# Performance work log

Hardware: AMD Instinct MI355X
Metric: run time of the kernel (lower is better)

Reference implementation:

```python
import jax, jax.numpy as jnp
import numpy as np

LEAK = 0.1
LOG_2PI = float(np.log(2.0 * np.pi))


def setup_inputs() -> dict:
    key = jax.random.key(0)
    k1, k2, k3, k4 = jax.random.split(key, 4)
    B, S, K = 128, 8192, 16
    obvs = jax.random.normal(k1, (B, S, 1), dtype=jnp.float32)
    mu = jax.random.normal(k2, (K,), dtype=jnp.float32)
    log_sigma = 0.1 * jax.random.normal(k3, (K,), dtype=jnp.float32)
    prior_logits = jax.random.normal(k4, (K,), dtype=jnp.float32)
    return {"obvs": obvs, "mu": mu, "log_sigma": log_sigma, "prior_logits": prior_logits}


def _log_transition(num_states: int) -> jnp.ndarray:
    # LeakyTransfer: diagonal-dominant stochastic matrix, stay prob 1-leak,
    # leak mass spread uniformly over the other K-1 states.
    eye = jnp.eye(num_states, dtype=jnp.float32)
    A = (1.0 - LEAK) * eye + (LEAK / (num_states - 1)) * (1.0 - eye)
    return jnp.log(A)


def reference(obvs, mu, log_sigma, prior_logits):
    K = mu.shape[0]
    # Gaussian emission NLL per state: [B, S, K]
    sigma = jnp.exp(log_sigma)
    nll = 0.5 * ((obvs - mu) / sigma) ** 2 + log_sigma + 0.5 * LOG_2PI
    ln_em = -nll  # ln_emission_probs

    log_prior = jax.nn.log_softmax(prior_logits)  # CategoricalPrior
    logA = _log_transition(K)  # [K, K] (from -> to)

    # forward recursion: carry[b, j] = ln_em[b, t, j] + logsumexp_i(carry[b, i] + logA[i, j])
    init = ln_em[:, 0, :] + log_prior  # [B, K]
    em_rest = jnp.swapaxes(ln_em[:, 1:, :], 0, 1)  # [S-1, B, K]

    def step(carry, em_t):
        trans = jax.nn.logsumexp(carry[:, :, None] + logA[None, :, :], axis=1)  # [B, K]
        carry = em_t + trans
        return carry, None

    final, _ = jax.lax.scan(step, init, em_rest)
    return jnp.sum(jax.nn.logsumexp(final, axis=-1))
```

## Files before the change

### kernel.cpp

```cpp
#include <hip/hip_runtime.h>

#define NB 128
#define NS 8192
#define NC 128
#define NCP 64
#define NL (NS / NC)
#define M4 (NL / 4)

#define LOG2E 1.4426950408889634f
#define HLOG2PI 0.918938533204672742f
#define LN2 0.69314718055994531f

#define ROWS 20
#define UNIT 640
#define SLOT 320

__device__ __forceinline__ float fexp2(float x) { return __builtin_amdgcn_exp2f(x); }
__device__ __forceinline__ float flog2(float x) { return __builtin_amdgcn_logf(x); }

__device__ __forceinline__ float gsum16(float v) {
    v += __shfl_xor(v, 1, 16);
    v += __shfl_xor(v, 2, 16);
    v += __shfl_xor(v, 4, 16);
    v += __shfl_xor(v, 8, 16);
    return v;
}
__device__ __forceinline__ float gmax16(float v) {
    v = fmaxf(v, __shfl_xor(v, 1, 16));
    v = fmaxf(v, __shfl_xor(v, 2, 16));
    v = fmaxf(v, __shfl_xor(v, 4, 16));
    v = fmaxf(v, __shfl_xor(v, 8, 16));
    return v;
}

template <int K>
__device__ __forceinline__ int rotk(int x) {
    return __builtin_amdgcn_mov_dpp(x, 0x120 + K, 0xF, 0xF, true);
}

__device__ __forceinline__ float step2(float (&W)[16], float T, float xx,
                                       float A2, float B2, float C2) {
    const float amb = 0.9f - 0.1f / 15.0f;
    const float bco = 0.1f / 15.0f;
    float myl = fexp2(fmaf(xx, fmaf(xx, A2, B2), C2));
    int mi = __float_as_int(myl);
    float bT = bco * T;
    W[0]  = fmaf(amb, W[0],  bT) * myl;
    W[1]  = fmaf(amb, W[1],  bT) * __int_as_float(rotk<1>(mi));
    W[2]  = fmaf(amb, W[2],  bT) * __int_as_float(rotk<2>(mi));
    W[3]  = fmaf(amb, W[3],  bT) * __int_as_float(rotk<3>(mi));
    W[4]  = fmaf(amb, W[4],  bT) * __int_as_float(rotk<4>(mi));
    W[5]  = fmaf(amb, W[5],  bT) * __int_as_float(rotk<5>(mi));
    W[6]  = fmaf(amb, W[6],  bT) * __int_as_float(rotk<6>(mi));
    W[7]  = fmaf(amb, W[7],  bT) * __int_as_float(rotk<7>(mi));
    W[8]  = fmaf(amb, W[8],  bT) * __int_as_float(rotk<8>(mi));
    W[9]  = fmaf(amb, W[9],  bT) * __int_as_float(rotk<9>(mi));
    W[10] = fmaf(amb, W[10], bT) * __int_as_float(rotk<10>(mi));
    W[11] = fmaf(amb, W[11], bT) * __int_as_float(rotk<11>(mi));
    W[12] = fmaf(amb, W[12], bT) * __int_as_float(rotk<12>(mi));
    W[13] = fmaf(amb, W[13], bT) * __int_as_float(rotk<13>(mi));
    W[14] = fmaf(amb, W[14], bT) * __int_as_float(rotk<14>(mi));
    W[15] = fmaf(amb, W[15], bT) * __int_as_float(rotk<15>(mi));
    float s0 = (W[0] + W[1]) + (W[2] + W[3]);
    float s1 = (W[4] + W[5]) + (W[6] + W[7]);
    float s2 = (W[8] + W[9]) + (W[10] + W[11]);
    float s3 = (W[12] + W[13]) + (W[14] + W[15]);
    return (s0 + s1) + (s2 + s3);
}

__global__ __launch_bounds__(256, 4) void hmm_phase1(const float* __restrict__ obvs,
                                                     const float* __restrict__ mu,
                                                     const float* __restrict__ log_sigma,
                                                     float* __restrict__ wsW,
                                                     float* __restrict__ wsM,
                                                     float* __restrict__ out) {
    __shared__ float lds[16 * UNIT];
    int tid = blockIdx.x * 256 + threadIdx.x;
    if (tid == 0) out[0] = 0.0f;
    int r = threadIdx.x & 15;
    int u = threadIdx.x >> 4;
    int g = tid >> 4;
    int b = g >> 7;
    int c = g & (NC - 1);

    float ls = log_sigma[r];
    float mk = mu[r];
    float iv = fexp2(-2.0f * LOG2E * ls);
    float A2 = -0.5f * LOG2E * iv;
    float B2 = LOG2E * mk * iv;
    float C2 = LOG2E * (-0.5f * mk * mk * iv - ls - HLOG2PI);

    float W[16];
#pragma unroll
    for (int k = 0; k < 16; ++k) W[k] = (k == 0) ? 1.0f : 0.0f;
    int ilog = 0;
    float T = 1.0f;

    const float4* ob4 = (const float4*)(obvs + (long)b * NS) + c * M4;
    float4 xv = ob4[0];
    float4 xn = ob4[1];
    if (c) T = step2(W, T, xv.x, A2, B2, C2);
    T = step2(W, T, xv.y, A2, B2, C2);
    T = step2(W, T, xv.z, A2, B2, C2);
    T = step2(W, T, xv.w, A2, B2, C2);
    {
        int te = (__float_as_int(T) >> 23) & 255;
        int ok = (te != 0);
        float s = ok ? __int_as_float((254 - te) << 23) : 1.0f;
        ilog += ok ? (te - 127) : 0;
#pragma unroll
        for (int k = 0; k < 16; ++k) W[k] *= s;
        T *= s;
    }
    xv = xn;
    for (int m = 1; m < M4; ++m) {
        xn = ob4[(m + 1) < M4 ? (m + 1) : m];
        T = step2(W, T, xv.x, A2, B2, C2);
        T = step2(W, T, xv.y, A2, B2, C2);
        T = step2(W, T, xv.z, A2, B2, C2);
        T = step2(W, T, xv.w, A2, B2, C2);
        int te = (__float_as_int(T) >> 23) & 255;
        int ok = (te != 0);
        float s = ok ? __int_as_float((254 - te) << 23) : 1.0f;
        ilog += ok ? (te - 127) : 0;
#pragma unroll
        for (int k = 0; k < 16; ++k) W[k] *= s;
        T *= s;
        xv = xn;
    }

    int sid[16];
    sid[0] = r;
    sid[1]  = rotk<1>(r);   sid[2]  = rotk<2>(r);   sid[3]  = rotk<3>(r);
    sid[4]  = rotk<4>(r);   sid[5]  = rotk<5>(r);   sid[6]  = rotk<6>(r);
    sid[7]  = rotk<7>(r);   sid[8]  = rotk<8>(r);   sid[9]  = rotk<9>(r);
    sid[10] = rotk<10>(r);  sid[11] = rotk<11>(r);  sid[12] = rotk<12>(r);
    sid[13] = rotk<13>(r);  sid[14] = rotk<14>(r);  sid[15] = rotk<15>(r);

    float lg = (float)ilog + flog2(T);
    float mx = gmax16(lg);
    float sc = fexp2((float)ilog - mx);

    float* Ru = lds + u * UNIT;
    float* Tu = lds + u * UNIT + SLOT;
#pragma unroll
    for (int k = 0; k < 16; ++k) {
        float w = W[k] * sc;
        int j = sid[k];
        Ru[j * ROWS + r] = w;
        Tu[r * ROWS + j] = w;
    }
    if (r == 0) Ru[16] = mx;
    __syncthreads();

    int lane = threadIdx.x & 63;
    int wid = threadIdx.x >> 6;
    long p0 = (long)blockIdx.x * 8;
#pragma unroll
    for (int q = 0; q < 2; ++q) {
        int p = 2 * wid + q;
        const float* MbR = lds + (2 * p + 1) * UNIT;
        const float* MaT = lds + (2 * p) * UNIT + SLOT;
        int a = lane >> 3, cc = lane & 7;
        float b0[16], b1[16], a0[16], a1[16];
        const float4* pb0 = (const float4*)(MbR + (2 * a) * ROWS);
        const float4* pb1 = (const float4*)(MbR + (2 * a + 1) * ROWS);
        const float4* pa0 = (const float4*)(MaT + (2 * cc) * ROWS);
        const float4* pa1 = (const float4*)(MaT + (2 * cc + 1) * ROWS);
#pragma unroll
        for (int qq = 0; qq < 4; ++qq) {
            *(float4*)&b0[4 * qq] = pb0[qq];
            *(float4*)&b1[4 * qq] = pb1[qq];
            *(float4*)&a0[4 * qq] = pa0[qq];
            *(float4*)&a1[4 * qq] = pa1[qq];
        }
        float c00 = 0.f, c01 = 0.f, c10 = 0.f, c11 = 0.f;
#pragma unroll
        for (int k = 0; k < 16; ++k) {
            c00 = fmaf(b0[k], a0[k], c00);
            c01 = fmaf(b0[k], a1[k], c01);
            c10 = fmaf(b1[k], a0[k], c10);
            c11 = fmaf(b1[k], a1[k], c11);
        }
        float cs0 = c00 + c10;
        float cs1 = c01 + c11;
        cs0 += __shfl_xor(cs0, 8);  cs1 += __shfl_xor(cs1, 8);
        cs0 += __shfl_xor(cs0, 16); cs1 += __shfl_xor(cs1, 16);
        cs0 += __shfl_xor(cs0, 32); cs1 += __shfl_xor(cs1, 32);
        float mxc = fmaxf(cs0, cs1);
        mxc = fmaxf(mxc, __shfl_xor(mxc, 1));
        mxc = fmaxf(mxc, __shfl_xor(mxc, 2));
        mxc = fmaxf(mxc, __shfl_xor(mxc, 4));
        float is = 1.0f / mxc;
        float* dst = wsW + (p0 + p) * 256;
        *(float2*)(dst + (2 * a) * 16 + 2 * cc)     = make_float2(c00 * is, c01 * is);
        *(float2*)(dst + (2 * a + 1) * 16 + 2 * cc) = make_float2(c10 * is, c11 * is);
        if (lane == 0) {
            float mxa = lds[(2 * p) * UNIT + 16];
            float mxb = lds[(2 * p + 1) * UNIT + 16];
            wsM[p0 + p] = mxa + mxb + flog2(mxc);
        }
    }
}

__device__ __forceinline__ void mat16_mul(float* dR, float* dT,
                                          const float* MbR, const float* MaT,
                                          int lane) {
    int a = lane >> 3;
    int cc = lane & 7;
    float b0[16], b1[16], a0[16], a1[16];
    const float4* pb0 = (const float4*)(MbR + (2 * a) * ROWS);
    const float4* pb1 = (const float4*)(MbR + (2 * a + 1) * ROWS);
    const float4* pa0 = (const float4*)(MaT + (2 * cc) * ROWS);
    const float4* pa1 = (const float4*)(MaT + (2 * cc + 1) * ROWS);
#pragma unroll
    for (int q = 0; q < 4; ++q) {
        *(float4*)&b0[4 * q] = pb0[q];
        *(float4*)&b1[4 * q] = pb1[q];
        *(float4*)&a0[4 * q] = pa0[q];
        *(float4*)&a1[4 * q] = pa1[q];
    }
    float c00 = 0.f, c01 = 0.f, c10 = 0.f, c11 = 0.f;
#pragma unroll
    for (int k = 0; k < 16; ++k) {
        c00 = fmaf(b0[k], a0[k], c00);
        c01 = fmaf(b0[k], a1[k], c01);
        c10 = fmaf(b1[k], a0[k], c10);
        c11 = fmaf(b1[k], a1[k], c11);
    }
    *(float2*)(dR + (2 * a) * ROWS + 2 * cc)     = make_float2(c00, c01);
    *(float2*)(dR + (2 * a + 1) * ROWS + 2 * cc) = make_float2(c10, c11);
    if (dT) {
        *(float2*)(dT + (2 * cc) * ROWS + 2 * a)     = make_float2(c00, c10);
        *(float2*)(dT + (2 * cc + 1) * ROWS + 2 * a) = make_float2(c01, c11);
    }
}

__global__ __launch_bounds__(256, 2) void hmm_phase23(const float* __restrict__ obvs,
                                                      const float* __restrict__ mu,
                                                      const float* __restrict__ log_sigma,
                                                      const float* __restrict__ prior_logits,
                                                      const float* __restrict__ wsW,
                                                      const float* __restrict__ wsM,
                                                      float* __restrict__ out) {
    __shared__ float smem[12800];
    float* stage = smem;
    float* scr   = smem + 5120;
    float* resB  = smem + 10240;

    int bb = blockIdx.x;
    int tid = threadIdx.x;
    int wid = tid >> 6;
    int lane = tid & 63;

    for (int rd = 0; rd < 8; ++rd) {
        const float4* src = (const float4*)(wsW + ((long)bb * NCP + rd * 8) * 256);
        __syncthreads();
#pragma unroll
        for (int q = 0; q < 2; ++q) {
            int f = tid + q * 256;
            float4 v = src[f];
            int m = f >> 6, idx = f & 63, j = idx >> 2, kq = idx & 3;
            *(float4*)(stage + m * UNIT + j * ROWS + kq * 4) = v;
            float* Tb = stage + m * UNIT + SLOT;
            Tb[(4 * kq + 0) * ROWS + j] = v.x;
            Tb[(4 * kq + 1) * ROWS + j] = v.y;
            Tb[(4 * kq + 2) * ROWS + j] = v.z;
            Tb[(4 * kq + 3) * ROWS + j] = v.w;
        }
        __syncthreads();
        if (wid < 4)
            mat16_mul(scr + wid * UNIT, scr + wid * UNIT + SLOT,
                      stage + (2 * wid + 1) * UNIT, stage + (2 * wid) * UNIT + SLOT, lane);
        __syncthreads();
        if (wid < 2)
            mat16_mul(scr + (4 + wid) * UNIT, scr + (4 + wid) * UNIT + SLOT,
                      scr + (2 * wid + 1) * UNIT, scr + (2 * wid) * UNIT + SLOT, lane);
        __syncthreads();
        if (wid == 0)
            mat16_mul(resB + rd * SLOT, nullptr,
                      scr + 5 * UNIT, scr + 4 * UNIT + SLOT, lane);
    }
    __syncthreads();

    for (int e = tid; e < 8 * 256; e += 256) {
        int m = e >> 8, idx = e & 255, j = idx >> 4, r = idx & 15;
        stage[m * SLOT + r * ROWS + j] = resB[m * SLOT + j * ROWS + r];
    }
    __syncthreads();

    for (int i = wid; i < 4; i += 4)
        mat16_mul(scr + i * UNIT, scr + i * UNIT + SLOT,
                  resB + (2 * i + 1) * SLOT, stage + (2 * i) * SLOT, lane);
    __syncthreads();
    float* cur = scr;
    float* oth = stage;
    int n = 4;
    while (n > 1) {
        n >>= 1;
        for (int i = wid; i < n; i += 4)
            mat16_mul(oth + i * UNIT, oth + i * UNIT + SLOT,
                      cur + (2 * i + 1) * UNIT, cur + (2 * i) * UNIT + SLOT, lane);
        __syncthreads();
        float* t = cur; cur = oth; oth = t;
    }

    if (tid < 16) {
        int jj = tid;
        float ls = log_sigma[jj];
        float mk = mu[jj];
        float iv = fexp2(-2.0f * LOG2E * ls);
        float A2 = -0.5f * LOG2E * iv;
        float B2 = LOG2E * mk * iv;
        float C2 = LOG2E * (-0.5f * mk * mk * iv - ls - HLOG2PI);
        float x = obvs[(long)bb * NS];
        float e = fexp2(LOG2E * prior_logits[jj]);
        float Z = gsum16(e);
        float p0 = fexp2(fmaf(x, fmaf(x, A2, B2), C2)) * e;
        const float* Mrow = cur + jj * ROWS;
        float mr[16];
        *(float4*)&mr[0]  = ((const float4*)Mrow)[0];
        *(float4*)&mr[4]  = ((const float4*)Mrow)[1];
        *(float4*)&mr[8]  = ((const float4*)Mrow)[2];
        *(float4*)&mr[12] = ((const float4*)Mrow)[3];
        float q = 0.0f;
#pragma unroll
        for (int rr = 0; rr < 16; ++rr) q = fmaf(mr[rr], __shfl(p0, rr, 16), q);
        float Tq = gsum16(q);
        const float* pm = wsM + bb * NCP + jj * 4;
        float msum = gsum16(pm[0] + pm[1] + pm[2] + pm[3]);
        if (jj == 0) {
            float res = (flog2(Tq) - flog2(Z) + msum) * LN2;
            atomicAdd(out, res);
        }
    }
}

extern "C" void kernel_launch(void* const* d_in, const int* in_sizes, int n_in,
                              void* d_out, int out_size, void* d_ws, size_t ws_size,
                              hipStream_t stream) {
    const float* obvs = (const float*)d_in[0];
    const float* mu = (const float*)d_in[1];
    const float* log_sigma = (const float*)d_in[2];
    const float* prior_logits = (const float*)d_in[3];
    float* out = (float*)d_out;

    float* wsW = (float*)d_ws;
    float* wsM = wsW + (size_t)NB * NCP * 256;

    hmm_phase1<<<dim3(NB * NC * 16 / 256), dim3(256), 0, stream>>>(obvs, mu, log_sigma,
                                                                   wsW, wsM, out);
    hmm_phase23<<<dim3(NB), dim3(256), 0, stream>>>(obvs, mu, log_sigma, prior_logits,
                                                    wsW, wsM, out);
}
```

Measured before the change: 106.4 us.

## Reduce full per-block matrix tree in phase1 to cut phase23 workload

Phase1 now combines all 16 per-chunk transition matrices within the block through a log-depth tree of normalized 16x16 products in LDS. Each block writes a single matrix and log-scale instead of eight, so the intermediate buffer shrinks from 64 to 8 matrices per batch. Phase23 then needs only one load round and a three-level tree, which removes most of its serial work and global traffic. The cost is extra syncthreads and idle waves in phase1's tree levels, and each level adds a renormalization step.

New measurement: 96.36 us. 1.1x faster.

```diff
diff --git a/kernel.cpp b/kernel.cpp
--- a/kernel.cpp
+++ b/kernel.cpp
@@ -3,7 +3,7 @@
 #define NB 128
 #define NS 8192
 #define NC 128
-#define NCP 64
+#define NCP 8
 #define NL (NS / NC)
 #define M4 (NL / 4)
 
@@ -68,6 +68,52 @@
     return (s0 + s1) + (s2 + s3);
 }
 
+__device__ __forceinline__ void combineUnits(float* lds, int ua, int ub, int ud, int lane) {
+    const float* MbR = lds + ub * UNIT;
+    const float* MaT = lds + ua * UNIT + SLOT;
+    float mxa = lds[ua * UNIT + 16];
+    float mxb = lds[ub * UNIT + 16];
+    int a = lane >> 3, cc = lane & 7;
+    float b0[16], b1[16], a0[16], a1[16];
+    const float4* pb0 = (const float4*)(MbR + (2 * a) * ROWS);
+    const float4* pb1 = (const float4*)(MbR + (2 * a + 1) * ROWS);
+    const float4* pa0 = (const float4*)(MaT + (2 * cc) * ROWS);
+    const float4* pa1 = (const float4*)(MaT + (2 * cc + 1) * ROWS);
+#pragma unroll
+    for (int q = 0; q < 4; ++q) {
+        *(float4*)&b0[4 * q] = pb0[q];
+        *(float4*)&b1[4 * q] = pb1[q];
+        *(float4*)&a0[4 * q] = pa0[q];
+        *(float4*)&a1[4 * q] = pa1[q];
+    }
+    float c00 = 0.f, c01 = 0.f, c10 = 0.f, c11 = 0.f;
+#pragma unroll
+    for (int k = 0; k < 16; ++k) {
+        c00 = fmaf(b0[k], a0[k], c00);
+        c01 = fmaf(b0[k], a1[k], c01);
+        c10 = fmaf(b1[k], a0[k], c10);
+        c11 = fmaf(b1[k], a1[k], c11);
+    }
+    float cs0 = c00 + c10;
+    float cs1 = c01 + c11;
+    cs0 += __shfl_xor(cs0, 8);  cs1 += __shfl_xor(cs1, 8);
+    cs0 += __shfl_xor(cs0, 16); cs1 += __shfl_xor(cs1, 16);
+    cs0 += __shfl_xor(cs0, 32); cs1 += __shfl_xor(cs1, 32);
+    float mxc = fmaxf(cs0, cs1);
+    mxc = fmaxf(mxc, __shfl_xor(mxc, 1));
+    mxc = fmaxf(mxc, __shfl_xor(mxc, 2));
+    mxc = fmaxf(mxc, __shfl_xor(mxc, 4));
+    float is = 1.0f / mxc;
+    c00 *= is; c01 *= is; c10 *= is; c11 *= is;
+    float* dR = lds + ud * UNIT;
+    float* dT = lds + ud * UNIT + SLOT;
+    *(float2*)(dR + (2 * a) * ROWS + 2 * cc)     = make_float2(c00, c01);
+    *(float2*)(dR + (2 * a + 1) * ROWS + 2 * cc) = make_float2(c10, c11);
+    *(float2*)(dT + (2 * cc) * ROWS + 2 * a)     = make_float2(c00, c10);
+    *(float2*)(dT + (2 * cc + 1) * ROWS + 2 * a) = make_float2(c01, c11);
+    if (lane == 0) lds[ud * UNIT + 16] = mxa + mxb + flog2(mxc);
+}
+
 __global__ __launch_bounds__(256, 4) void hmm_phase1(const float* __restrict__ obvs,
                                                      const float* __restrict__ mu,
                                                      const float* __restrict__ log_sigma,
@@ -155,52 +201,22 @@
 
     int lane = threadIdx.x & 63;
     int wid = threadIdx.x >> 6;
-    long p0 = (long)blockIdx.x * 8;
 #pragma unroll
     for (int q = 0; q < 2; ++q) {
         int p = 2 * wid + q;
-        const float* MbR = lds + (2 * p + 1) * UNIT;
-        const float* MaT = lds + (2 * p) * UNIT + SLOT;
-        int a = lane >> 3, cc = lane & 7;
-        float b0[16], b1[16], a0[16], a1[16];
-        const float4* pb0 = (const float4*)(MbR + (2 * a) * ROWS);
-        const float4* pb1 = (const float4*)(MbR + (2 * a + 1) * ROWS);
-        const float4* pa0 = (const float4*)(MaT + (2 * cc) * ROWS);
-        const float4* pa1 = (const float4*)(MaT + (2 * cc + 1) * ROWS);
-#pragma unroll
-        for (int qq = 0; qq < 4; ++qq) {
-            *(float4*)&b0[4 * qq] = pb0[qq];
-            *(float4*)&b1[4 * qq] = pb1[qq];
-            *(float4*)&a0[4 * qq] = pa0[qq];
-            *(float4*)&a1[4 * qq] = pa1[qq];
-        }
-        float c00 = 0.f, c01 = 0.f, c10 = 0.f, c11 = 0.f;
-#pragma unroll
-        for (int k = 0; k < 16; ++k) {
-            c00 = fmaf(b0[k], a0[k], c00);
-            c01 = fmaf(b0[k], a1[k], c01);
-            c10 = fmaf(b1[k], a0[k], c10);
-            c11 = fmaf(b1[k], a1[k], c11);
-        }
-        float cs0 = c00 + c10;
-        float cs1 = c01 + c11;
-        cs0 += __shfl_xor(cs0, 8);  cs1 += __shfl_xor(cs1, 8);
-        cs0 += __shfl_xor(cs0, 16); cs1 += __shfl_xor(cs1, 16);
-        cs0 += __shfl_xor(cs0, 32); cs1 += __shfl_xor(cs1, 32);
-        float mxc = fmaxf(cs0, cs1);
-        mxc = fmaxf(mxc, __shfl_xor(mxc, 1));
-        mxc = fmaxf(mxc, __shfl_xor(mxc, 2));
-        mxc = fmaxf(mxc, __shfl_xor(mxc, 4));
-        float is = 1.0f / mxc;
-        float* dst = wsW + (p0 + p) * 256;
-        *(float2*)(dst + (2 * a) * 16 + 2 * cc)     = make_float2(c00 * is, c01 * is);
-        *(float2*)(dst + (2 * a + 1) * 16 + 2 * cc) = make_float2(c10 * is, c11 * is);
-        if (lane == 0) {
-            float mxa = lds[(2 * p) * UNIT + 16];
-            float mxb = lds[(2 * p + 1) * UNIT + 16];
-            wsM[p0 + p] = mxa + mxb + flog2(mxc);
-        }
-    }
+        combineUnits(lds, 2 * p, 2 * p + 1, 2 * p, lane);
+    }
+    __syncthreads();
+    if (wid < 4) combineUnits(lds, 4 * wid, 4 * wid + 2, 4 * wid, lane);
+    __syncthreads();
+    if (wid < 2) combineUnits(lds, 8 * wid, 8 * wid + 4, 8 * wid, lane);
+    __syncthreads();
+    if (wid == 0) combineUnits(lds, 0, 8, 0, lane);
+    __syncthreads();
+
+    wsW[(long)blockIdx.x * 256 + threadIdx.x] =
+        lds[(threadIdx.x >> 4) * ROWS + (threadIdx.x & 15)];
+    if (threadIdx.x == 0) wsM[blockIdx.x] = lds[16];
 }
 
 __device__ __forceinline__ void mat16_mul(float* dR, float* dT,
@@ -243,7 +259,7 @@
                                                       const float* __restrict__ wsW,
                                                       const float* __restrict__ wsM,
                                                       float* __restrict__ out) {
-    __shared__ float smem[12800];
+    __shared__ float smem[10560];
     float* stage = smem;
     float* scr   = smem + 5120;
     float* resB  = smem + 10240;
@@ -253,57 +269,31 @@
     int wid = tid >> 6;
     int lane = tid & 63;
 
-    for (int rd = 0; rd < 8; ++rd) {
-        const float4* src = (const float4*)(wsW + ((long)bb * NCP + rd * 8) * 256);
-        __syncthreads();
-#pragma unroll
-        for (int q = 0; q < 2; ++q) {
-            int f = tid + q * 256;
-            float4 v = src[f];
-            int m = f >> 6, idx = f & 63, j = idx >> 2, kq = idx & 3;
-            *(float4*)(stage + m * UNIT + j * ROWS + kq * 4) = v;
-            float* Tb = stage + m * UNIT + SLOT;
-            Tb[(4 * kq + 0) * ROWS + j] = v.x;
-            Tb[(4 * kq + 1) * ROWS + j] = v.y;
-            Tb[(4 * kq + 2) * ROWS + j] = v.z;
-            Tb[(4 * kq + 3) * ROWS + j] = v.w;
-        }
-        __syncthreads();
-        if (wid < 4)
-            mat16_mul(scr + wid * UNIT, scr + wid * UNIT + SLOT,
-                      stage + (2 * wid + 1) * UNIT, stage + (2 * wid) * UNIT + SLOT, lane);
-        __syncthreads();
-        if (wid < 2)
-            mat16_mul(scr + (4 + wid) * UNIT, scr + (4 + wid) * UNIT + SLOT,
-                      scr + (2 * wid + 1) * UNIT, scr + (2 * wid) * UNIT + SLOT, lane);
-        __syncthreads();
-        if (wid == 0)
-            mat16_mul(resB + rd * SLOT, nullptr,
-                      scr + 5 * UNIT, scr + 4 * UNIT + SLOT, lane);
-    }
-    __syncthreads();
-
-    for (int e = tid; e < 8 * 256; e += 256) {
-        int m = e >> 8, idx = e & 255, j = idx >> 4, r = idx & 15;
-        stage[m * SLOT + r * ROWS + j] = resB[m * SLOT + j * ROWS + r];
-    }
-    __syncthreads();
-
-    for (int i = wid; i < 4; i += 4)
-        mat16_mul(scr + i * UNIT, scr + i * UNIT + SLOT,
-                  resB + (2 * i + 1) * SLOT, stage + (2 * i) * SLOT, lane);
-    __syncthreads();
-    float* cur = scr;
-    float* oth = stage;
-    int n = 4;
-    while (n > 1) {
-        n >>= 1;
-        for (int i = wid; i < n; i += 4)
-            mat16_mul(oth + i * UNIT, oth + i * UNIT + SLOT,
-                      cur + (2 * i + 1) * UNIT, cur + (2 * i) * UNIT + SLOT, lane);
-        __syncthreads();
-        float* t = cur; cur = oth; oth = t;
-    }
+    const float4* src = (const float4*)(wsW + (long)bb * NCP * 256);
+#pragma unroll
+    for (int q = 0; q < 2; ++q) {
+        int f = tid + q * 256;
+        float4 v = src[f];
+        int m = f >> 6, idx = f & 63, j = idx >> 2, kq = idx & 3;
+        *(float4*)(stage + m * UNIT + j * ROWS + kq * 4) = v;
+        float* Tb = stage + m * UNIT + SLOT;
+        Tb[(4 * kq + 0) * ROWS + j] = v.x;
+        Tb[(4 * kq + 1) * ROWS + j] = v.y;
+        Tb[(4 * kq + 2) * ROWS + j] = v.z;
+        Tb[(4 * kq + 3) * ROWS + j] = v.w;
+    }
+    __syncthreads();
+    if (wid < 4)
+        mat16_mul(scr + wid * UNIT, scr + wid * UNIT + SLOT,
+                  stage + (2 * wid + 1) * UNIT, stage + (2 * wid) * UNIT + SLOT, lane);
+    __syncthreads();
+    if (wid < 2)
+        mat16_mul(scr + (4 + wid) * UNIT, scr + (4 + wid) * UNIT + SLOT,
+                  scr + (2 * wid + 1) * UNIT, scr + (2 * wid) * UNIT + SLOT, lane);
+    __syncthreads();
+    if (wid == 0)
+        mat16_mul(resB, nullptr, scr + 5 * UNIT, scr + 4 * UNIT + SLOT, lane);
+    __syncthreads();
 
     if (tid < 16) {
         int jj = tid;
@@ -317,7 +307,7 @@
         float e = fexp2(LOG2E * prior_logits[jj]);
         float Z = gsum16(e);
         float p0 = fexp2(fmaf(x, fmaf(x, A2, B2), C2)) * e;
-        const float* Mrow = cur + jj * ROWS;
+        const float* Mrow = resB + jj * ROWS;
         float mr[16];
         *(float4*)&mr[0]  = ((const float4*)Mrow)[0];
         *(float4*)&mr[4]  = ((const float4*)Mrow)[1];
@@ -327,8 +317,8 @@
 #pragma unroll
         for (int rr = 0; rr < 16; ++rr) q = fmaf(mr[rr], __shfl(p0, rr, 16), q);
         float Tq = gsum16(q);
-        const float* pm = wsM + bb * NCP + jj * 4;
-        float msum = gsum16(pm[0] + pm[1] + pm[2] + pm[3]);
+        float pm = (jj < NCP) ? wsM[bb * NCP + jj] : 0.0f;
+        float msum = gsum16(pm);
         if (jj == 0) {
             float res = (flog2(Tq) - flog2(Z) + msum) * LN2;
             atomicAdd(out, res);
```
